# Optimization experiments

Measured on AMD Instinct MI355X. Metric: run time of the kernel, lower is better.

Reference implementation:

```python
import jax, jax.numpy as jnp
import numpy as np

TOP_K = 2
CAPACITY_FACTOR = 1.25
AUX_LOSS_ALPHA = 0.01
Z_LOSS_ALPHA = 0.001


def setup_inputs() -> dict:
    key = jax.random.key(0)
    k1, k2, k3, k4 = jax.random.split(key, 4)
    B, S, H, I, E = 4, 2048, 1024, 4096, 8
    x = jax.random.normal(k1, (B, S, H), dtype=jnp.float32)
    # router: xavier_uniform with gain 0.1
    router_w = jax.random.normal(k2, (H, E), dtype=jnp.float32) * 0.1 * (2.0 / (H + E)) ** 0.5
    # expert weights: kaiming-ish scale 1/sqrt(fan_in)
    w1 = jax.random.normal(k3, (E, H, I), dtype=jnp.float32) * (1.0 / H) ** 0.5
    w2 = jax.random.normal(k4, (E, I, H), dtype=jnp.float32) * (1.0 / I) ** 0.5
    return {"x": x, "router_w": router_w, "w1": w1, "w2": w2}


def reference(x, router_w, w1, w2):
    B, S, H = x.shape
    E = router_w.shape[1]
    # router logits [B, S, E]
    logits = jnp.einsum('bsh,he->bse', x, router_w)
    # expert-choice: each expert picks `capacity` tokens along the seq axis
    capacity = int(min(S, max(1, (S * TOP_K) // E * CAPACITY_FACTOR)))
    topk_vals, topk_idx = jax.lax.top_k(jnp.swapaxes(logits, 1, 2), capacity)  # [B, E, C]
    topk_w = jax.nn.softmax(topk_vals, axis=-1)  # [B, E, C]
    # flat indices into [B*S] token space
    flat_idx = (jnp.arange(B)[:, None, None] * S + topk_idx).reshape(-1)  # [B*E*C]
    x_flat = x.reshape(-1, H)
    selected = x_flat[flat_idx].reshape(B, E, capacity, H)
    # per-expert SiLU MLP as grouped GEMMs
    mid = jax.nn.silu(jnp.einsum('bech,ehi->beci', selected, w1))
    expert_out = jnp.einsum('beci,eih->bech', mid, w2)
    weighted = (expert_out * topk_w[..., None]).reshape(-1, H)
    # scatter-add combine + count-based averaging
    out = jnp.zeros_like(x_flat).at[flat_idx].add(weighted)
    counts = jnp.zeros((B * S,), dtype=x.dtype).at[flat_idx].add(jnp.ones_like(flat_idx, dtype=x.dtype))
    out = (out / jnp.clip(counts, 1.0)[:, None]).reshape(B, S, H)
    # routing loss: load-balance aux + z-loss
    probs = jax.nn.softmax(logits, axis=-1)
    usage = probs.mean(axis=(0, 1))  # [E]
    aux_loss = jnp.mean((usage - 1.0 / E) ** 2) * E
    z_loss = jnp.mean(logits ** 2)
    routing_loss = AUX_LOSS_ALPHA * aux_loss + Z_LOSS_ALPHA * z_loss
    return out, routing_loss
```

## Files before the change

kernel.cpp:

```cpp
#include <hip/hip_runtime.h>
#include <hip/hip_bf16.h>
#include <stdint.h>

#define B_ 4
#define S_ 2048
#define H_ 1024
#define I_ 4096
#define E_ 8
#define CAP 640
#define NTOK (B_*S_)
#define NBE  (B_*E_)

typedef _Float16 f16;
typedef f16 f16x8 __attribute__((ext_vector_type(8)));
typedef float f32x4 __attribute__((ext_vector_type(4)));

#define OFF_LOGITS 0u
#define OFF_TOPKI  (256u*1024u)
#define OFF_TOPKW  (OFF_TOPKI + 128u*1024u)
#define OFF_COUNTS (OFF_TOPKW + 128u*1024u)
#define OFF_SCAL   (OFF_COUNTS + 64u*1024u)
#define OFF_XH     (1u<<20)
#define OFF_WT     (18u<<20)
#define OFF_MID    (86u<<20)

__device__ __forceinline__ void gl_lds16(const void* g, void* l) {
    __builtin_amdgcn_global_load_lds(
        (const __attribute__((address_space(1))) uint32_t*)g,
        (__attribute__((address_space(3))) uint32_t*)l, 16, 0, 0);
}

__global__ void k_router(const float* __restrict__ x, const float* __restrict__ rw,
                         float* __restrict__ logits, float* __restrict__ scal) {
    __shared__ float rwt[E_ * H_];
    __shared__ float part[4][9];
    int tid = threadIdx.x;
    for (int i = tid; i < E_ * H_; i += 256) {
        int h = i >> 3, e = i & 7;
        rwt[e * H_ + h] = rw[i];
    }
    __syncthreads();
    int w = tid >> 6, lane = tid & 63;
    int t = blockIdx.x * 4 + w;
    const float* xr = x + (size_t)t * H_;
    float acc[E_];
#pragma unroll
    for (int e = 0; e < E_; ++e) acc[e] = 0.f;
    for (int it = 0; it < H_ / 64; ++it) {
        int h = lane + it * 64;
        float xv = xr[h];
#pragma unroll
        for (int e = 0; e < E_; ++e) acc[e] += xv * rwt[e * H_ + h];
    }
#pragma unroll
    for (int off = 32; off > 0; off >>= 1)
#pragma unroll
        for (int e = 0; e < E_; ++e) acc[e] += __shfl_down(acc[e], off);
    if (lane == 0) {
        int b = t >> 11, s = t & 2047;
        float m = acc[0];
#pragma unroll
        for (int e = 1; e < E_; ++e) m = fmaxf(m, acc[e]);
        float z = 0.f, ps = 0.f;
        float p[E_];
#pragma unroll
        for (int e = 0; e < E_; ++e) {
            logits[(size_t)((b << 3) + e) * S_ + s] = acc[e];
            z += acc[e] * acc[e];
            p[e] = expf(acc[e] - m);
            ps += p[e];
        }
        part[w][0] = z;
#pragma unroll
        for (int e = 0; e < E_; ++e) part[w][1 + e] = p[e] / ps;
    }
    __syncthreads();
    if (tid < 9) {
        float v = part[0][tid] + part[1][tid] + part[2][tid] + part[3][tid];
        atomicAdd(&scal[tid], v);
    }
}

__global__ void __launch_bounds__(1024) k_topk(const float* __restrict__ logits,
                                               int* __restrict__ tki,
                                               float* __restrict__ tkw,
                                               float* __restrict__ counts) {
    int be = blockIdx.x;
    const float* row = logits + (size_t)be * S_;
    __shared__ unsigned long long keys[S_];
    __shared__ float wpart[16];
    __shared__ float stot;
    int tid = threadIdx.x;
    for (int i = tid; i < S_; i += 1024) {
        unsigned u = __float_as_uint(row[i]);
        u = (u & 0x80000000u) ? ~u : (u | 0x80000000u);
        keys[i] = ((unsigned long long)u << 32) | (unsigned)(~i);
    }
    __syncthreads();
    for (int k = 2; k <= S_; k <<= 1) {
        for (int j = k >> 1; j > 0; j >>= 1) {
#pragma unroll
            for (int base = 0; base < S_; base += 1024) {
                int i = base + tid;
                int ixj = i ^ j;
                if (ixj > i) {
                    unsigned long long a = keys[i], b = keys[ixj];
                    bool up = ((i & k) == 0);
                    bool sw = up ? (a < b) : (a > b);
                    if (sw) { keys[i] = b; keys[ixj] = a; }
                }
            }
            __syncthreads();
        }
    }
    int idx0 = (int)(~(unsigned)(keys[0] & 0xFFFFFFFFu));
    float vmax = row[idx0];
    int myidx = 0; float ex = 0.f;
    if (tid < CAP) {
        myidx = (int)(~(unsigned)(keys[tid] & 0xFFFFFFFFu));
        ex = expf(row[myidx] - vmax);
    }
    float v = ex;
#pragma unroll
    for (int off = 32; off > 0; off >>= 1) v += __shfl_down(v, off);
    if ((tid & 63) == 0) wpart[tid >> 6] = v;
    __syncthreads();
    if (tid == 0) {
        float s = 0.f;
#pragma unroll
        for (int i = 0; i < 16; ++i) s += wpart[i];
        stot = s;
    }
    __syncthreads();
    if (tid < CAP) {
        tki[be * CAP + tid] = myidx;
        tkw[be * CAP + tid] = ex / stot;
        atomicAdd(&counts[(be >> 3) * S_ + myidx], 1.0f);
    }
}

__global__ void k_cvt_x(const float* __restrict__ in, f16* __restrict__ out) {
    size_t i = ((size_t)blockIdx.x * 256 + threadIdx.x) << 3;
    float4 a = *(const float4*)(in + i);
    float4 b = *(const float4*)(in + i + 4);
    f16x8 o = { (f16)a.x, (f16)a.y, (f16)a.z, (f16)a.w,
                (f16)b.x, (f16)b.y, (f16)b.z, (f16)b.w };
    *(f16x8*)(out + i) = o;
}

template<int R, int C>
__global__ void __launch_bounds__(256) k_transpose(const float* __restrict__ in,
                                                   f16* __restrict__ out) {
    __shared__ f16 t[64][68];
    int e = blockIdx.z;
    const float* ine = in + (size_t)e * R * C;
    f16* oute = out + (size_t)e * R * C;
    int c0 = blockIdx.x << 6, r0 = blockIdx.y << 6;
    int tx = threadIdx.x & 15, ty = threadIdx.x >> 4;
#pragma unroll
    for (int p = 0; p < 4; ++p) {
        int r = ty + p * 16;
        float4 v = *(const float4*)(ine + (size_t)(r0 + r) * C + c0 + tx * 4);
        t[tx * 4 + 0][r] = (f16)v.x;
        t[tx * 4 + 1][r] = (f16)v.y;
        t[tx * 4 + 2][r] = (f16)v.z;
        t[tx * 4 + 3][r] = (f16)v.w;
    }
    __syncthreads();
#pragma unroll
    for (int p = 0; p < 4; ++p) {
        int c = ty + p * 16;
        *(ushort4*)(oute + (size_t)(c0 + c) * R + r0 + tx * 4) =
            *(const ushort4*)&t[c][tx * 4];
    }
}


#define MFMA4(MI, A) \
    acc[MI][0] = __builtin_amdgcn_mfma_f32_16x16x32_f16(A, bf0, acc[MI][0], 0, 0, 0); \
    acc[MI][1] = __builtin_amdgcn_mfma_f32_16x16x32_f16(A, bf1, acc[MI][1], 0, 0, 0); \
    acc[MI][2] = __builtin_amdgcn_mfma_f32_16x16x32_f16(A, bf2, acc[MI][2], 0, 0, 0); \
    acc[MI][3] = __builtin_amdgcn_mfma_f32_16x16x32_f16(A, bf3, acc[MI][3], 0, 0, 0);

__global__ void __launch_bounds__(256, 4) k_gemm1(const f16* __restrict__ xh,
                                                  const f16* __restrict__ w1t,
                                                  const int* __restrict__ tki,
                                                  f16* __restrict__ mid) {
    __shared__ f16 As[128 * 64];
    __shared__ f16 Bs[128 * 64];
    int bid = blockIdx.x;
    int e = bid & 7;
    int r = bid >> 3;
    int rt = r % 20;
    int ct = r / 20;
    int n0 = ct << 7;
    const f16* w1e = w1t + ((size_t)e << 22);
    int tid = threadIdx.x;
    int w = tid >> 6, l = tid & 63;
    int wm = w >> 1, wn = w & 1;

    int gch = (tid & 7) ^ ((tid >> 3) & 7);
    int dstb = (tid >> 6) << 9;
    const f16* aS[4];
    const f16* bS[4];
#pragma unroll
    for (int i = 0; i < 4; ++i) {
        int ri = i * 32 + (tid >> 3);
        int ge = rt * 128 + ri;
        int bb = ge / 640;
        int cc = ge - bb * 640;
        int tok = tki[((bb << 3) + e) * 640 + cc];
        aS[i] = xh + ((size_t)((bb << 11) + tok) << 10) + (gch << 3);
        bS[i] = w1e + ((size_t)(n0 + ri) << 10) + (gch << 3);
    }

    int fr = l & 15, c4 = l >> 4;
    int f7 = fr & 7;
    int arow = (wm << 6) + fr;
    int brow = (wn << 6) + fr;
    f32x4 acc[4][4];
#pragma unroll
    for (int mi = 0; mi < 4; ++mi)
#pragma unroll
        for (int ni = 0; ni < 4; ++ni) acc[mi][ni] = (f32x4){0.f, 0.f, 0.f, 0.f};

    const int NT = H_ / 64;
    for (int t = 0; t < NT; ++t) {
        int ko = t << 6;
#pragma unroll
        for (int i = 0; i < 4; ++i) {
            gl_lds16(aS[i] + ko, As + i * 2048 + dstb);
            gl_lds16(bS[i] + ko, Bs + i * 2048 + dstb);
        }
        __syncthreads();
#pragma unroll
        for (int kf = 0; kf < 2; ++kf) {
            int sl = (((kf << 2) | c4) ^ f7) << 3;
            f16x8 bf0 = *(const f16x8*)(Bs + brow * 64 + sl);
            f16x8 bf1 = *(const f16x8*)(Bs + (brow + 16) * 64 + sl);
            f16x8 bf2 = *(const f16x8*)(Bs + (brow + 32) * 64 + sl);
            f16x8 bf3 = *(const f16x8*)(Bs + (brow + 48) * 64 + sl);
            f16x8 a0 = *(const f16x8*)(As + arow * 64 + sl);
            f16x8 a1 = *(const f16x8*)(As + (arow + 16) * 64 + sl);
            f16x8 a2 = *(const f16x8*)(As + (arow + 32) * 64 + sl);
            f16x8 a3 = *(const f16x8*)(As + (arow + 48) * 64 + sl);
            MFMA4(0, a0) MFMA4(1, a1) MFMA4(2, a2) MFMA4(3, a3)
        }
        __syncthreads();
    }

    int rq4 = c4 << 2;
#pragma unroll
    for (int mi = 0; mi < 4; ++mi) {
#pragma unroll
        for (int q = 0; q < 4; ++q) {
            int row = (wm << 6) + mi * 16 + rq4 + q;
            int ge = rt * 128 + row;
            int bb = ge / 640;
            int cc = ge - bb * 640;
            size_t flat = (size_t)(((bb << 3) + e) * 640 + cc);
            f16* mrow = mid + (flat << 12) + n0 + (wn << 6) + fr;
#pragma unroll
            for (int ni = 0; ni < 4; ++ni) {
                float v = acc[mi][ni][q];
                v = v / (1.f + expf(-v));
                mrow[ni * 16] = (f16)v;
            }
        }
    }
}

__global__ void __launch_bounds__(256, 4) k_gemm2(const f16* __restrict__ mid,
                                                  const f16* __restrict__ w2t,
                                                  const int* __restrict__ tki,
                                                  const float* __restrict__ tkw,
                                                  float* __restrict__ out) {
    __shared__ f16 As[128 * 64];
    __shared__ f16 Bs[128 * 64];
    __shared__ int   rowOffS[128];
    __shared__ float wtsS[128];
    int bid = blockIdx.x;
    int e = bid & 7;
    int r = bid >> 3;
    int rt = r % 20;
    int ct = r / 20;
    int n0 = ct << 7;
    const f16* w2e = w2t + ((size_t)e << 22);
    int tid = threadIdx.x;
    int w = tid >> 6, l = tid & 63;
    int wm = w >> 1, wn = w & 1;

    if (tid < 128) {
        int ge = rt * 128 + tid;
        int bb = ge / 640;
        int cc = ge - bb * 640;
        int flat = ((bb << 3) + e) * 640 + cc;
        int tok = tki[flat];
        rowOffS[tid] = ((bb << 11) + tok) << 10;
        wtsS[tid] = tkw[flat];
    }

    int gch = (tid & 7) ^ ((tid >> 3) & 7);
    int dstb = (tid >> 6) << 9;
    const f16* aS[4];
    const f16* bS[4];
#pragma unroll
    for (int i = 0; i < 4; ++i) {
        int ri = i * 32 + (tid >> 3);
        int ge = rt * 128 + ri;
        int bb = ge / 640;
        int cc = ge - bb * 640;
        size_t flat = (size_t)(((bb << 3) + e) * 640 + cc);
        aS[i] = mid + (flat << 12) + (gch << 3);
        bS[i] = w2e + ((size_t)(n0 + ri) << 12) + (gch << 3);
    }

    int fr = l & 15, c4 = l >> 4;
    int f7 = fr & 7;
    int arow = (wm << 6) + fr;
    int brow = (wn << 6) + fr;
    f32x4 acc[4][4];
#pragma unroll
    for (int mi = 0; mi < 4; ++mi)
#pragma unroll
        for (int ni = 0; ni < 4; ++ni) acc[mi][ni] = (f32x4){0.f, 0.f, 0.f, 0.f};

    const int NT = I_ / 64;
    for (int t = 0; t < NT; ++t) {
        int ko = t << 6;
#pragma unroll
        for (int i = 0; i < 4; ++i) {
            gl_lds16(aS[i] + ko, As + i * 2048 + dstb);
            gl_lds16(bS[i] + ko, Bs + i * 2048 + dstb);
        }
        __syncthreads();
#pragma unroll
        for (int kf = 0; kf < 2; ++kf) {
            int sl = (((kf << 2) | c4) ^ f7) << 3;
            f16x8 bf0 = *(const f16x8*)(Bs + brow * 64 + sl);
            f16x8 bf1 = *(const f16x8*)(Bs + (brow + 16) * 64 + sl);
            f16x8 bf2 = *(const f16x8*)(Bs + (brow + 32) * 64 + sl);
            f16x8 bf3 = *(const f16x8*)(Bs + (brow + 48) * 64 + sl);
            f16x8 a0 = *(const f16x8*)(As + arow * 64 + sl);
            f16x8 a1 = *(const f16x8*)(As + (arow + 16) * 64 + sl);
            f16x8 a2 = *(const f16x8*)(As + (arow + 32) * 64 + sl);
            f16x8 a3 = *(const f16x8*)(As + (arow + 48) * 64 + sl);
            MFMA4(0, a0) MFMA4(1, a1) MFMA4(2, a2) MFMA4(3, a3)
        }
        __syncthreads();
    }

    int rq4 = c4 << 2;
#pragma unroll
    for (int mi = 0; mi < 4; ++mi) {
#pragma unroll
        for (int q = 0; q < 4; ++q) {
            int row = (wm << 6) + mi * 16 + rq4 + q;
            int ro = rowOffS[row] + n0 + (wn << 6) + fr;
            float wg = wtsS[row];
#pragma unroll
            for (int ni = 0; ni < 4; ++ni) {
                atomicAdd(&out[ro + ni * 16], acc[mi][ni][q] * wg);
            }
        }
    }
}

__global__ void k_final(float* __restrict__ out, const float* __restrict__ counts,
                        const float* __restrict__ scal, float* __restrict__ loss_out) {
    size_t gid = (size_t)blockIdx.x * 256 + threadIdx.x;
    int tok = (int)(gid >> 8);
    float c = fmaxf(counts[tok], 1.0f);
    float4* o4 = (float4*)out;
    float4 v = o4[gid];
    v.x /= c; v.y /= c; v.z /= c; v.w /= c;
    o4[gid] = v;
    if (gid == 0) {
        float z = scal[0] / (float)(NTOK * E_);
        float aux = 0.f;
#pragma unroll
        for (int e = 0; e < E_; ++e) {
            float u = scal[1 + e] / (float)NTOK - 0.125f;
            aux += u * u;
        }
        loss_out[0] = 0.01f * aux + 0.001f * z;
    }
}

extern "C" void kernel_launch(void* const* d_in, const int* in_sizes, int n_in,
                              void* d_out, int out_size, void* d_ws, size_t ws_size,
                              hipStream_t stream) {
    const float* x  = (const float*)d_in[0];
    const float* rw = (const float*)d_in[1];
    const float* w1 = (const float*)d_in[2];
    const float* w2 = (const float*)d_in[3];
    float* out = (float*)d_out;
    char* ws = (char*)d_ws;

    float* logits = (float*)(ws + OFF_LOGITS);
    int*   tki    = (int*)(ws + OFF_TOPKI);
    float* tkw    = (float*)(ws + OFF_TOPKW);
    float* counts = (float*)(ws + OFF_COUNTS);
    float* scal   = (float*)(ws + OFF_SCAL);
    f16*   xh     = (f16*)(ws + OFF_XH);
    f16*   wt     = (f16*)(ws + OFF_WT);
    f16*   mid    = (f16*)(ws + OFF_MID);

    hipMemsetAsync(ws + OFF_COUNTS, 0, 64u * 1024u + 64u, stream);
    hipMemsetAsync(d_out, 0, (size_t)out_size * sizeof(float), stream);

    k_cvt_x<<<NTOK * H_ / 8 / 256, 256, 0, stream>>>(x, xh);
    k_transpose<H_, I_><<<dim3(I_ / 64, H_ / 64, E_), 256, 0, stream>>>(w1, wt);
    k_router<<<NTOK / 4, 256, 0, stream>>>(x, rw, logits, scal);
    k_topk<<<NBE, 1024, 0, stream>>>(logits, tki, tkw, counts);
    k_gemm1<<<5120, 256, 0, stream>>>(xh, wt, tki, mid);
    k_transpose<I_, H_><<<dim3(H_ / 64, I_ / 64, E_), 256, 0, stream>>>(w2, wt);
    k_gemm2<<<1280, 256, 0, stream>>>(mid, wt, tki, tkw, out);
    k_final<<<(NTOK * H_ / 4) / 256, 256, 0, stream>>>(out, counts, scal,
                                                       out + (size_t)NTOK * H_);
}
```

Before: 605.4 us.

## Replace bitonic top-k with radix select, fuse x conversion into router

The top-k kernel now uses an 8-pass byte radix select to find the capacity threshold instead of a full bitonic sort in shared memory. Selected tokens are written through an atomic slot counter, so their order within each expert is no longer sorted. The fp16 conversion of x moves into the router kernel, which removes a separate pass over x. The GEMM launch bounds rise to 5 waves per SIMD, and gemm2 drops its shared-memory staging of row offsets and weights in favour of direct global loads in the epilogue.

```diff
diff --git a/kernel.cpp b/kernel.cpp
--- a/kernel.cpp
+++ b/kernel.cpp
@@ -31,7 +31,8 @@
 }
 
 __global__ void k_router(const float* __restrict__ x, const float* __restrict__ rw,
-                         float* __restrict__ logits, float* __restrict__ scal) {
+                         float* __restrict__ logits, float* __restrict__ scal,
+                         f16* __restrict__ xh) {
     __shared__ float rwt[E_ * H_];
     __shared__ float part[4][9];
     int tid = threadIdx.x;
@@ -43,12 +44,14 @@
     int w = tid >> 6, lane = tid & 63;
     int t = blockIdx.x * 4 + w;
     const float* xr = x + (size_t)t * H_;
+    f16* xhr = xh + ((size_t)t << 10);
     float acc[E_];
 #pragma unroll
     for (int e = 0; e < E_; ++e) acc[e] = 0.f;
     for (int it = 0; it < H_ / 64; ++it) {
         int h = lane + it * 64;
         float xv = xr[h];
+        xhr[h] = (f16)xv;
 #pragma unroll
         for (int e = 0; e < E_; ++e) acc[e] += xv * rwt[e * H_ + h];
     }
@@ -87,65 +90,121 @@
                                                float* __restrict__ counts) {
     int be = blockIdx.x;
     const float* row = logits + (size_t)be * S_;
-    __shared__ unsigned long long keys[S_];
-    __shared__ float wpart[16];
-    __shared__ float stot;
+    __shared__ unsigned hist[256];
+    __shared__ unsigned long long wmax[16];
+    __shared__ float wsum[16];
+    __shared__ unsigned long long sh_prefix;
+    __shared__ unsigned sh_rem;
+    __shared__ unsigned long long sh_max;
+    __shared__ float sh_stot;
+    __shared__ unsigned sh_cnt;
     int tid = threadIdx.x;
-    for (int i = tid; i < S_; i += 1024) {
-        unsigned u = __float_as_uint(row[i]);
-        u = (u & 0x80000000u) ? ~u : (u | 0x80000000u);
-        keys[i] = ((unsigned long long)u << 32) | (unsigned)(~i);
-    }
-    __syncthreads();
-    for (int k = 2; k <= S_; k <<= 1) {
-        for (int j = k >> 1; j > 0; j >>= 1) {
-#pragma unroll
-            for (int base = 0; base < S_; base += 1024) {
-                int i = base + tid;
-                int ixj = i ^ j;
-                if (ixj > i) {
-                    unsigned long long a = keys[i], b = keys[ixj];
-                    bool up = ((i & k) == 0);
-                    bool sw = up ? (a < b) : (a > b);
-                    if (sw) { keys[i] = b; keys[ixj] = a; }
+
+    unsigned u0 = __float_as_uint(row[tid]);
+    u0 = (u0 & 0x80000000u) ? ~u0 : (u0 | 0x80000000u);
+    unsigned long long k0 = ((unsigned long long)u0 << 32) | (unsigned)(~tid);
+    unsigned u1 = __float_as_uint(row[tid + 1024]);
+    u1 = (u1 & 0x80000000u) ? ~u1 : (u1 | 0x80000000u);
+    unsigned long long k1 = ((unsigned long long)u1 << 32) | (unsigned)(~(tid + 1024));
+
+    if (tid == 0) { sh_cnt = 0; sh_rem = CAP; sh_prefix = 0; }
+    unsigned long long m = k0 > k1 ? k0 : k1;
+#pragma unroll
+    for (int off = 32; off > 0; off >>= 1) {
+        unsigned long long o = __shfl_down(m, off);
+        if (o > m) m = o;
+    }
+    if ((tid & 63) == 0) wmax[tid >> 6] = m;
+    __syncthreads();
+    if (tid == 0) {
+        unsigned long long mm = wmax[0];
+#pragma unroll
+        for (int i = 1; i < 16; ++i) if (wmax[i] > mm) mm = wmax[i];
+        sh_max = mm;
+    }
+
+    unsigned long long prefix = 0;
+    for (int L = 0; L < 8; ++L) {
+        int shift = 56 - 8 * L;
+        if (tid < 256) hist[tid] = 0;
+        __syncthreads();
+        bool m0 = (L == 0) || (((k0 ^ prefix) >> (shift + 8)) == 0);
+        if (m0) atomicAdd(&hist[(unsigned)((k0 >> shift) & 255)], 1u);
+        bool m1 = (L == 0) || (((k1 ^ prefix) >> (shift + 8)) == 0);
+        if (m1) atomicAdd(&hist[(unsigned)((k1 >> shift) & 255)], 1u);
+        __syncthreads();
+        if (tid < 64) {
+            unsigned g0 = hist[tid * 4], g1 = hist[tid * 4 + 1];
+            unsigned g2 = hist[tid * 4 + 2], g3 = hist[tid * 4 + 3];
+            unsigned gs = g0 + g1 + g2 + g3;
+            unsigned suf = gs;
+#pragma unroll
+            for (int off = 1; off < 64; off <<= 1) {
+                unsigned o = __shfl_down(suf, off);
+                if (tid + off < 64) suf += o;
+            }
+            unsigned remaining = sh_rem;
+            unsigned before = suf - gs;
+            if (before < remaining && remaining <= suf) {
+                unsigned cum = before;
+                int bsel = tid * 4;
+                unsigned rem2 = 0;
+                for (int b = tid * 4 + 3; b >= tid * 4; --b) {
+                    unsigned h = hist[b];
+                    cum += h;
+                    if (cum >= remaining) { bsel = b; rem2 = remaining - (cum - h); break; }
                 }
+                sh_prefix = prefix | ((unsigned long long)(unsigned)bsel << shift);
+                sh_rem = rem2;
             }
-            __syncthreads();
-        }
-    }
-    int idx0 = (int)(~(unsigned)(keys[0] & 0xFFFFFFFFu));
-    float vmax = row[idx0];
-    int myidx = 0; float ex = 0.f;
-    if (tid < CAP) {
-        myidx = (int)(~(unsigned)(keys[tid] & 0xFFFFFFFFu));
-        ex = expf(row[myidx] - vmax);
-    }
-    float v = ex;
-#pragma unroll
-    for (int off = 32; off > 0; off >>= 1) v += __shfl_down(v, off);
-    if ((tid & 63) == 0) wpart[tid >> 6] = v;
+        }
+        __syncthreads();
+        prefix = sh_prefix;
+    }
+    unsigned long long T = prefix;
+
+    unsigned vu = (unsigned)(sh_max >> 32);
+    float vmax = __uint_as_float((vu & 0x80000000u) ? (vu ^ 0x80000000u) : ~vu);
+
+    float ex0 = 0.f, ex1 = 0.f;
+    int idx0 = 0, idx1 = 0;
+    if (k0 >= T) {
+        idx0 = (int)(~(unsigned)k0) & 2047;
+        unsigned vb = (unsigned)(k0 >> 32);
+        float v = __uint_as_float((vb & 0x80000000u) ? (vb ^ 0x80000000u) : ~vb);
+        ex0 = expf(v - vmax);
+    }
+    if (k1 >= T) {
+        idx1 = (int)(~(unsigned)k1) & 2047;
+        unsigned vb = (unsigned)(k1 >> 32);
+        float v = __uint_as_float((vb & 0x80000000u) ? (vb ^ 0x80000000u) : ~vb);
+        ex1 = expf(v - vmax);
+    }
+    float s = ex0 + ex1;
+#pragma unroll
+    for (int off = 32; off > 0; off >>= 1) s += __shfl_down(s, off);
+    if ((tid & 63) == 0) wsum[tid >> 6] = s;
     __syncthreads();
     if (tid == 0) {
-        float s = 0.f;
-#pragma unroll
-        for (int i = 0; i < 16; ++i) s += wpart[i];
-        stot = s;
-    }
-    __syncthreads();
-    if (tid < CAP) {
-        tki[be * CAP + tid] = myidx;
-        tkw[be * CAP + tid] = ex / stot;
-        atomicAdd(&counts[(be >> 3) * S_ + myidx], 1.0f);
-    }
-}
-
-__global__ void k_cvt_x(const float* __restrict__ in, f16* __restrict__ out) {
-    size_t i = ((size_t)blockIdx.x * 256 + threadIdx.x) << 3;
-    float4 a = *(const float4*)(in + i);
-    float4 b = *(const float4*)(in + i + 4);
-    f16x8 o = { (f16)a.x, (f16)a.y, (f16)a.z, (f16)a.w,
-                (f16)b.x, (f16)b.y, (f16)b.z, (f16)b.w };
-    *(f16x8*)(out + i) = o;
+        float t2 = 0.f;
+#pragma unroll
+        for (int i = 0; i < 16; ++i) t2 += wsum[i];
+        sh_stot = t2;
+    }
+    __syncthreads();
+    float stot = sh_stot;
+    if (k0 >= T) {
+        unsigned slot = atomicAdd(&sh_cnt, 1u);
+        tki[be * CAP + slot] = idx0;
+        tkw[be * CAP + slot] = ex0 / stot;
+        atomicAdd(&counts[(be >> 3) * S_ + idx0], 1.0f);
+    }
+    if (k1 >= T) {
+        unsigned slot = atomicAdd(&sh_cnt, 1u);
+        tki[be * CAP + slot] = idx1;
+        tkw[be * CAP + slot] = ex1 / stot;
+        atomicAdd(&counts[(be >> 3) * S_ + idx1], 1.0f);
+    }
 }
 
 template<int R, int C>
@@ -182,7 +241,7 @@
     acc[MI][2] = __builtin_amdgcn_mfma_f32_16x16x32_f16(A, bf2, acc[MI][2], 0, 0, 0); \
     acc[MI][3] = __builtin_amdgcn_mfma_f32_16x16x32_f16(A, bf3, acc[MI][3], 0, 0, 0);
 
-__global__ void __launch_bounds__(256, 4) k_gemm1(const f16* __restrict__ xh,
+__global__ void __launch_bounds__(256, 5) k_gemm1(const f16* __restrict__ xh,
                                                   const f16* __restrict__ w1t,
                                                   const int* __restrict__ tki,
                                                   f16* __restrict__ mid) {
@@ -270,15 +329,13 @@
     }
 }
 
-__global__ void __launch_bounds__(256, 4) k_gemm2(const f16* __restrict__ mid,
+__global__ void __launch_bounds__(256, 5) k_gemm2(const f16* __restrict__ mid,
                                                   const f16* __restrict__ w2t,
                                                   const int* __restrict__ tki,
                                                   const float* __restrict__ tkw,
                                                   float* __restrict__ out) {
     __shared__ f16 As[128 * 64];
     __shared__ f16 Bs[128 * 64];
-    __shared__ int   rowOffS[128];
-    __shared__ float wtsS[128];
     int bid = blockIdx.x;
     int e = bid & 7;
     int r = bid >> 3;
@@ -289,16 +346,6 @@
     int tid = threadIdx.x;
     int w = tid >> 6, l = tid & 63;
     int wm = w >> 1, wn = w & 1;
-
-    if (tid < 128) {
-        int ge = rt * 128 + tid;
-        int bb = ge / 640;
-        int cc = ge - bb * 640;
-        int flat = ((bb << 3) + e) * 640 + cc;
-        int tok = tki[flat];
-        rowOffS[tid] = ((bb << 11) + tok) << 10;
-        wtsS[tid] = tkw[flat];
-    }
 
     int gch = (tid & 7) ^ ((tid >> 3) & 7);
     int dstb = (tid >> 6) << 9;
@@ -356,11 +403,16 @@
 #pragma unroll
         for (int q = 0; q < 4; ++q) {
             int row = (wm << 6) + mi * 16 + rq4 + q;
-            int ro = rowOffS[row] + n0 + (wn << 6) + fr;
-            float wg = wtsS[row];
+            int ge = rt * 128 + row;
+            int bb = ge / 640;
+            int cc = ge - bb * 640;
+            int flat = ((bb << 3) + e) * 640 + cc;
+            int tok = tki[flat];
+            float wg = tkw[flat];
+            float* orow = out + (((size_t)((bb << 11) + tok)) << 10) + n0 + (wn << 6) + fr;
 #pragma unroll
             for (int ni = 0; ni < 4; ++ni) {
-                atomicAdd(&out[ro + ni * 16], acc[mi][ni][q] * wg);
+                atomicAdd(&orow[ni * 16], acc[mi][ni][q] * wg);
             }
         }
     }
@@ -409,9 +461,8 @@
     hipMemsetAsync(ws + OFF_COUNTS, 0, 64u * 1024u + 64u, stream);
     hipMemsetAsync(d_out, 0, (size_t)out_size * sizeof(float), stream);
 
-    k_cvt_x<<<NTOK * H_ / 8 / 256, 256, 0, stream>>>(x, xh);
     k_transpose<H_, I_><<<dim3(I_ / 64, H_ / 64, E_), 256, 0, stream>>>(w1, wt);
-    k_router<<<NTOK / 4, 256, 0, stream>>>(x, rw, logits, scal);
+    k_router<<<NTOK / 4, 256, 0, stream>>>(x, rw, logits, scal, xh);
     k_topk<<<NBE, 1024, 0, stream>>>(logits, tki, tkw, counts);
     k_gemm1<<<5120, 256, 0, stream>>>(xh, wt, tki, mid);
     k_transpose<I_, H_><<<dim3(H_ / 64, I_ / 64, E_), 256, 0, stream>>>(w2, wt);
```

New measurement: 905.1 us. +49.5%, slower.
